# Kernel tuning notes

Measured on AMD Instinct MI355X. Metric: run time of the kernel, lower is better.

The kernel has to match this reference:

```python
import jax, jax.numpy as jnp
import numpy as np

N_NODES = 50000
N_EDGES = 800000
UNITS = 64
NUM_RADIAL = 20


def setup_inputs() -> dict:
    key = jax.random.key(0)
    ks = jax.random.split(key, 12)
    u, r = UNITS, NUM_RADIAL
    inv_u = 1.0 / np.sqrt(u)
    inv_r = 1.0 / np.sqrt(r)
    return {
        "node": jax.random.normal(ks[0], (N_NODES, u), jnp.float32),
        "equivariant": jax.random.normal(ks[1], (N_NODES, 3, u), jnp.float32),
        "rbf": jax.random.uniform(ks[2], (N_EDGES, r), jnp.float32),
        "envelope": jax.random.uniform(ks[3], (N_EDGES, 1), jnp.float32),
        "r_ij": jax.random.normal(ks[4], (N_EDGES, 3), jnp.float32),
        "edge_index": jax.random.randint(ks[5], (N_EDGES, 2), 0, N_NODES, jnp.int64),
        "Ws": jax.random.uniform(ks[6], (u, u), jnp.float32, -inv_u, inv_u),
        "bs": jax.random.uniform(ks[7], (u,), jnp.float32, -inv_u, inv_u),
        "Wphi": jax.random.uniform(ks[8], (3 * u, u), jnp.float32, -inv_u, inv_u),
        "bphi": jax.random.uniform(ks[9], (3 * u,), jnp.float32, -inv_u, inv_u),
        "Ww": jax.random.uniform(ks[10], (3 * u, r), jnp.float32, -inv_r, inv_r),
        "bw": jax.random.uniform(ks[11], (3 * u,), jnp.float32, -inv_r, inv_r),
    }


def reference(node, equivariant, rbf, envelope, r_ij, edge_index,
              Ws, bs, Wphi, bphi, Ww, bw):
    n_nodes = node.shape[0]
    u = node.shape[1]
    # per-node dense projections
    s = jax.nn.silu(node @ Ws.T + bs)          # [N, u]
    s = s @ Wphi.T + bphi                      # [N, 3u]
    # gather to edges (source = column 1)
    s_e = s[edge_index[:, 1]]                  # [E, 3u]
    # per-edge radial filter with cutoff envelope
    w = rbf @ Ww.T + bw                        # [E, 3u]
    w = w * envelope
    sw = s_e * w                               # [E, 3u]
    sw1, sw2, sw3 = jnp.split(sw, 3, axis=-1)  # each [E, u]
    dst = edge_index[:, 0]
    ds = jax.ops.segment_sum(sw1, dst, num_segments=n_nodes)  # [N, u]
    vj = equivariant[edge_index[:, 1]]         # [E, 3, u]
    dv = vj * sw2[:, None, :] + r_ij[:, :, None] * sw3[:, None, :]  # [E, 3, u]
    dv = jax.ops.segment_sum(dv, dst, num_segments=n_nodes)   # [N, 3, u]
    return (ds, dv)
```

## Files before the change

### kernel.cpp

```cpp
#include <hip/hip_runtime.h>

#define NRAD 20
#define MNODE 8

typedef unsigned short ushort_t;
typedef unsigned int uint_t;

struct U3 { uint_t a, b, c; };

__device__ __forceinline__ float rdlane(float v, int l)
{
    return __uint_as_float(__builtin_amdgcn_readlane(__float_as_uint(v), l));
}

__device__ __forceinline__ ushort_t f2bf(float f)
{
    uint_t u = __float_as_uint(f);
    u += 0x7fff + ((u >> 16) & 1);
    return (ushort_t)(u >> 16);
}

__device__ __forceinline__ uint_t pack2bf(float a, float b)
{
    return (uint_t)f2bf(a) | ((uint_t)f2bf(b) << 16);
}

__device__ __forceinline__ float bflo(uint_t w) { return __uint_as_float(w << 16); }
__device__ __forceinline__ float bfhi(uint_t w) { return __uint_as_float(w & 0xffff0000u); }
__device__ __forceinline__ float bf2f(ushort_t h) { return __uint_as_float(((uint_t)h) << 16); }

__global__ void detect_idx_kernel(const int* __restrict__ eidx, int* __restrict__ flag)
{
    int t = threadIdx.x;
    unsigned long long m = __ballot(eidx[2 * t + 1] != 0);
    if (t == 0) flag[0] = (__popcll(m) > 8) ? 1 : 0;
}

__global__ void hist_kernel(const int* __restrict__ eidx, const int* __restrict__ flag,
                            int* __restrict__ counts, int n_edges)
{
    int fmt32 = flag[0];
    int i0 = blockIdx.x * blockDim.x + threadIdx.x;
    int stride = gridDim.x * blockDim.x;
    if (fmt32) {
        for (int e = i0; e < n_edges; e += stride) atomicAdd(&counts[eidx[2 * e]], 1);
    } else {
        const long long* e64 = (const long long*)eidx;
        for (int e = i0; e < n_edges; e += stride) atomicAdd(&counts[(int)e64[2 * e]], 1);
    }
}

__global__ __launch_bounds__(256)
void scan1_kernel(const int* __restrict__ cnt, int* __restrict__ bsum, int n, int ch)
{
    __shared__ int red[4];
    int b = blockIdx.x, t = threadIdx.x;
    int end = min(n, (b + 1) * ch);
    int v = 0;
    for (int i = b * ch + t; i < end; i += 256) v += cnt[i];
#pragma unroll
    for (int d = 1; d < 64; d <<= 1) v += __shfl_xor(v, d, 64);
    if ((t & 63) == 0) red[t >> 6] = v;
    __syncthreads();
    if (t == 0) bsum[b] = red[0] + red[1] + red[2] + red[3];
}

__global__ __launch_bounds__(256)
void scan2_kernel(const int* __restrict__ bsum, int* __restrict__ bscan, int nb)
{
    __shared__ int wsum[4];
    int t = threadIdx.x, lane = t & 63, w = t >> 6;
    int v = (t < nb) ? bsum[t] : 0;
    int sc = v;
#pragma unroll
    for (int d = 1; d < 64; d <<= 1) {
        int u = __shfl_up(sc, (unsigned)d, 64);
        if (lane >= d) sc += u;
    }
    if (lane == 63) wsum[w] = sc;
    __syncthreads();
    int add = 0;
    for (int j = 0; j < w; j++) add += wsum[j];
    if (t < nb) bscan[t] = (sc + add) - v;
}

__global__ __launch_bounds__(256)
void scan3_kernel(const int* __restrict__ cnt, const int* __restrict__ bscan,
                  int* __restrict__ cur, int n, int ch)
{
    __shared__ int wsum[4];
    __shared__ int btot;
    int b = blockIdx.x, t = threadIdx.x, lane = t & 63, w = t >> 6;
    int end = min(n, (b + 1) * ch);
    int carry = bscan[b];
    for (int base = b * ch; base < end; base += 256) {
        int i = base + t;
        int v = (i < end) ? cnt[i] : 0;
        int sc = v;
#pragma unroll
        for (int d = 1; d < 64; d <<= 1) {
            int u = __shfl_up(sc, (unsigned)d, 64);
            if (lane >= d) sc += u;
        }
        if (lane == 63) wsum[w] = sc;
        __syncthreads();
        int add = 0;
        for (int j = 0; j < w; j++) add += wsum[j];
        if (t == 255) btot = sc + add;
        int excl = carry + (sc + add - v);
        if (i < end) cur[i] = excl;
        __syncthreads();
        carry += btot;
    }
}

__global__ void scatter_rec_kernel(const int* __restrict__ eidx, const int* __restrict__ flag,
                                   int* __restrict__ cur,
                                   const float* __restrict__ env, const float* __restrict__ rij,
                                   const float* __restrict__ rbf,
                                   uint4* __restrict__ rec, int n_edges)
{
    int fmt32 = flag[0];
    int i0 = blockIdx.x * blockDim.x + threadIdx.x;
    int stride = gridDim.x * blockDim.x;
    const long long* e64 = (const long long*)eidx;
    const float4* rbf4 = (const float4*)rbf;
    for (int e = i0; e < n_edges; e += stride) {
        int dst, src;
        if (fmt32) { dst = eidx[2 * e]; src = eidx[2 * e + 1]; }
        else       { dst = (int)e64[2 * e]; src = (int)e64[2 * e + 1]; }
        int pos = atomicAdd(&cur[dst], 1);
        float ev = env[e];
        float r0 = rij[3 * e], r1 = rij[3 * e + 1], r2 = rij[3 * e + 2];
        float4 b0 = rbf4[(size_t)e * 5 + 0];
        float4 b1 = rbf4[(size_t)e * 5 + 1];
        float4 b2 = rbf4[(size_t)e * 5 + 2];
        float4 b3 = rbf4[(size_t)e * 5 + 3];
        float4 b4 = rbf4[(size_t)e * 5 + 4];
        uint4 qa, qb, qc, qd;
        qa.x = (uint_t)src; qa.y = (uint_t)dst;
        qa.z = __float_as_uint(ev); qa.w = __float_as_uint(r0);
        qb.x = __float_as_uint(r1); qb.y = __float_as_uint(r2);
        qb.z = pack2bf(b0.x, b0.y); qb.w = pack2bf(b0.z, b0.w);
        qc.x = pack2bf(b1.x, b1.y); qc.y = pack2bf(b1.z, b1.w);
        qc.z = pack2bf(b2.x, b2.y); qc.w = pack2bf(b2.z, b2.w);
        qd.x = pack2bf(b3.x, b3.y); qd.y = pack2bf(b3.z, b3.w);
        qd.z = pack2bf(b4.x, b4.y); qd.w = pack2bf(b4.z, b4.w);
        size_t rp = (size_t)pos * 4;
        rec[rp] = qa; rec[rp + 1] = qb; rec[rp + 2] = qc; rec[rp + 3] = qd;
    }
}

__global__ void scatter_kernel(const int* __restrict__ eidx, const int* __restrict__ flag,
                               int* __restrict__ cur, int* __restrict__ sorted, int n_edges)
{
    int fmt32 = flag[0];
    int i0 = blockIdx.x * blockDim.x + threadIdx.x;
    int stride = gridDim.x * blockDim.x;
    const long long* e64 = (const long long*)eidx;
    for (int e = i0; e < n_edges; e += stride) {
        int dst = fmt32 ? eidx[2 * e] : (int)e64[2 * e];
        int pos = atomicAdd(&cur[dst], 1);
        sorted[pos] = e;
    }
}

__global__ void eq_cast_i_kernel(const float* __restrict__ eq,
                                 ushort_t* __restrict__ sq, int n_nodes)
{
    int i0 = blockIdx.x * blockDim.x + threadIdx.x;
    int stride = gridDim.x * blockDim.x;
    int total = n_nodes * 192;
    for (int i = i0; i < total; i += stride) {
        int n = i / 192;
        int r = i - n * 192;
        int c = r >> 6, ch = r & 63;
        sq[(size_t)n * 384 + ch * 6 + 3 + c] = f2bf(eq[i]);
    }
}

__global__ void prep_wpkp_kernel(const float* __restrict__ Ww, uint_t* __restrict__ wpkp)
{
    int idx = blockIdx.x * 256 + threadIdx.x;
    if (idx >= 1920) return;
    int lane = idx & 63;
    int r = idx >> 6;
    int p = r % 10;
    int c = r / 10;
    int n = c * 64 + lane;
    wpkp[idx] = pack2bf(Ww[n * 20 + 2 * p], Ww[n * 20 + 2 * p + 1]);
}

__global__ __launch_bounds__(256)
void node_mlp3i(const float* __restrict__ node,
                const float* __restrict__ Ws, const float* __restrict__ bs,
                const float* __restrict__ Wphi, const float* __restrict__ bphi,
                ushort_t* __restrict__ sq, int n_nodes)
{
    __shared__ float WsT[64 * 64];
    __shared__ float WphiT[64 * 192];
    const int t = threadIdx.x;
    for (int i = t; i < 64 * 64; i += 256) {
        int j = i >> 6, k = i & 63;
        WsT[k * 64 + j] = Ws[i];
    }
    for (int i = t; i < 192 * 64; i += 256) {
        int j = i >> 6, k = i & 63;
        WphiT[k * 192 + j] = Wphi[i];
    }
    __syncthreads();

    const int lane = t & 63;
    const int wave = t >> 6;
    const int gw = blockIdx.x * 4 + wave;
    const int nw = gridDim.x * 4;
    const float bsc = bs[lane];
    const float bp0 = bphi[lane], bp1 = bphi[64 + lane], bp2 = bphi[128 + lane];

    for (int n0 = gw * MNODE; n0 < n_nodes; n0 += nw * MNODE) {
        const int cnt = min(MNODE, n_nodes - n0);
        float x[MNODE];
#pragma unroll
        for (int m = 0; m < MNODE; m++)
            x[m] = (m < cnt) ? node[(size_t)(n0 + m) * 64 + lane] : 0.f;

        float acc[MNODE];
#pragma unroll
        for (int m = 0; m < MNODE; m++) acc[m] = bsc;
#pragma unroll
        for (int k = 0; k < 64; k++) {
            float wv = WsT[k * 64 + lane];
#pragma unroll
            for (int m = 0; m < MNODE; m++) acc[m] += rdlane(x[m], k) * wv;
        }
        float s1[MNODE];
#pragma unroll
        for (int m = 0; m < MNODE; m++) {
            float a = acc[m];
            s1[m] = a / (1.f + __expf(-a));
        }
        float a0[MNODE], a1[MNODE], a2[MNODE];
#pragma unroll
        for (int m = 0; m < MNODE; m++) { a0[m] = bp0; a1[m] = bp1; a2[m] = bp2; }
#pragma unroll
        for (int k = 0; k < 64; k++) {
            float w0 = WphiT[k * 192 + lane];
            float w1 = WphiT[k * 192 + 64 + lane];
            float w2 = WphiT[k * 192 + 128 + lane];
#pragma unroll
            for (int m = 0; m < MNODE; m++) {
                float sv = rdlane(s1[m], k);
                a0[m] += sv * w0;
                a1[m] += sv * w1;
                a2[m] += sv * w2;
            }
        }
#pragma unroll
        for (int m = 0; m < MNODE; m++) {
            if (m < cnt) {
                size_t ob = (size_t)(n0 + m) * 384 + lane * 6;
                *(uint_t*)(sq + ob) = pack2bf(a0[m], a1[m]);
                sq[ob + 2] = f2bf(a2[m]);
            }
        }
    }
}

__global__ __launch_bounds__(256, 4)
void accum10_kernel(const ushort_t* __restrict__ sq,
                    const uint4* __restrict__ rec,
                    const uint_t* __restrict__ wpkp,
                    const float* __restrict__ bw,
                    float* __restrict__ ds, float* __restrict__ dv, int n_edges)
{
    __shared__ int    sh_dst[4 * 64];
    __shared__ int    sh_src[4 * 64];
    __shared__ float  sh_env[4 * 64];
    __shared__ float  sh_r[4 * 3 * 64];
    __shared__ float4 sh_rbf[4 * 64 * 5];

    const int lane = threadIdx.x & 63;
    const int w = threadIdx.x >> 6;
    const int tile = blockIdx.x * 4 + w;
    const int base = tile * 64;
    const int nvalid = min(64, n_edges - base);
    const int woff = w * 64;

    uint_t wp[30];
#pragma unroll
    for (int i = 0; i < 30; i++) wp[i] = wpkp[i * 64 + lane];

    if (lane < nvalid) {
        size_t rp = (size_t)(base + lane) * 4;
        uint4 qa = rec[rp], qb = rec[rp + 1], qc = rec[rp + 2], qd = rec[rp + 3];
        sh_src[woff + lane] = (int)qa.x;
        sh_dst[woff + lane] = (int)qa.y;
        sh_env[woff + lane] = __uint_as_float(qa.z);
        sh_r[w * 192 + lane]       = __uint_as_float(qa.w);
        sh_r[w * 192 + 64 + lane]  = __uint_as_float(qb.x);
        sh_r[w * 192 + 128 + lane] = __uint_as_float(qb.y);
        float4* dstq = &sh_rbf[(woff + lane) * 5];
        dstq[0] = make_float4(bflo(qb.z), bfhi(qb.z), bflo(qb.w), bfhi(qb.w));
        dstq[1] = make_float4(bflo(qc.x), bfhi(qc.x), bflo(qc.y), bfhi(qc.y));
        dstq[2] = make_float4(bflo(qc.z), bfhi(qc.z), bflo(qc.w), bfhi(qc.w));
        dstq[3] = make_float4(bflo(qd.x), bfhi(qd.x), bflo(qd.y), bfhi(qd.y));
        dstq[4] = make_float4(bflo(qd.z), bfhi(qd.z), bflo(qd.w), bfhi(qd.w));
    }
    __syncthreads();

    if (nvalid <= 0) return;

    const float bw0 = bw[lane], bw1 = bw[64 + lane], bw2 = bw[128 + lane];

    float a0 = 0.f, a1 = 0.f, a2 = 0.f, a3 = 0.f;
    int cur = sh_dst[woff];

    U3 gcur = *(const U3*)(sq + (size_t)sh_src[woff] * 384 + lane * 6);

    for (int j = 0; j < nvalid; j++) {
        int jn = (j + 1 < nvalid) ? j + 1 : j;
        U3 gnxt = *(const U3*)(sq + (size_t)sh_src[woff + jn] * 384 + lane * 6);

        float ev = sh_env[woff + j];
        float r0 = sh_r[w * 192 + j];
        float r1 = sh_r[w * 192 + 64 + j];
        float r2 = sh_r[w * 192 + 128 + j];

        float sv0 = bflo(gcur.a);
        float sv1 = bfhi(gcur.a);
        float sv2 = bflo(gcur.b);
        float v0  = bfhi(gcur.b);
        float v1  = bflo(gcur.c);
        float v2  = bfhi(gcur.c);

        float w0 = bw0, w1 = bw1, w2 = bw2;
#pragma unroll
        for (int q = 0; q < 5; q++) {
            float4 rb = sh_rbf[(woff + j) * 5 + q];
            uint_t wa0 = wp[2 * q],      wa1 = wp[2 * q + 1];
            uint_t wb0 = wp[10 + 2 * q], wb1 = wp[11 + 2 * q];
            uint_t wc0 = wp[20 + 2 * q], wc1 = wp[21 + 2 * q];
            w0 += rb.x * bflo(wa0) + rb.y * bfhi(wa0) + rb.z * bflo(wa1) + rb.w * bfhi(wa1);
            w1 += rb.x * bflo(wb0) + rb.y * bfhi(wb0) + rb.z * bflo(wb1) + rb.w * bfhi(wb1);
            w2 += rb.x * bflo(wc0) + rb.y * bfhi(wc0) + rb.z * bflo(wc1) + rb.w * bfhi(wc1);
        }
        w0 *= ev; w1 *= ev; w2 *= ev;

        float sw1 = sv1 * w1;
        float sw2 = sv2 * w2;
        a0 += sv0 * w0;
        a1 += v0 * sw1 + r0 * sw2;
        a2 += v1 * sw1 + r1 * sw2;
        a3 += v2 * sw1 + r2 * sw2;

        int nd = (j + 1 < nvalid) ? sh_dst[woff + j + 1] : -2;
        if (nd != cur) {
            unsafeAtomicAdd(&ds[(size_t)cur * 64 + lane], a0);
            size_t db = (size_t)cur * 192 + lane;
            unsafeAtomicAdd(&dv[db], a1);
            unsafeAtomicAdd(&dv[db + 64], a2);
            unsafeAtomicAdd(&dv[db + 128], a3);
            a0 = a1 = a2 = a3 = 0.f;
            cur = nd;
        }
        gcur = gnxt;
    }
}

__global__ __launch_bounds__(256, 2)
void node_mlp_kernel(const float* __restrict__ node,
                     const float* __restrict__ Ws,
                     const float* __restrict__ bs,
                     const float* __restrict__ Wphi,
                     const float* __restrict__ bphi,
                     float* __restrict__ s_out,
                     int n_nodes)
{
    __shared__ float WsT[64 * 65];
    __shared__ float WphiT[64 * 193];
    const int t = threadIdx.x;
    for (int i = t; i < 64 * 64; i += 256) {
        int c = i >> 6, k = i & 63;
        WsT[k * 65 + c] = Ws[i];
    }
    for (int i = t; i < 192 * 64; i += 256) {
        int j = i >> 6, k = i & 63;
        WphiT[k * 193 + j] = Wphi[i];
    }
    __syncthreads();

    const int lane = t & 63;
    const int wave = t >> 6;
    const int nwaves = (gridDim.x * blockDim.x) >> 6;
    const float bsc = bs[lane];
    const float bp0 = bphi[lane], bp1 = bphi[64 + lane], bp2 = bphi[128 + lane];

    for (int n = blockIdx.x * 4 + wave; n < n_nodes; n += nwaves) {
        float x = node[(size_t)n * 64 + lane];
        float acc = bsc;
#pragma unroll
        for (int k = 0; k < 64; k++) acc += __shfl(x, k) * WsT[k * 65 + lane];
        float s1 = acc / (1.0f + __expf(-acc));
        float a0 = bp0, a1 = bp1, a2 = bp2;
#pragma unroll
        for (int k = 0; k < 64; k++) {
            float sk = __shfl(s1, k);
            a0 += sk * WphiT[k * 193 + lane];
            a1 += sk * WphiT[k * 193 + 64 + lane];
            a2 += sk * WphiT[k * 193 + 128 + lane];
        }
        size_t ob = (size_t)n * 192;
        s_out[ob + lane] = a0;
        s_out[ob + 64 + lane] = a1;
        s_out[ob + 128 + lane] = a2;
    }
}

__global__ __launch_bounds__(256)
void edge_kernel(const float* __restrict__ s,
                 const float* __restrict__ eq,
                 const float* __restrict__ rbf,
                 const float* __restrict__ env,
                 const float* __restrict__ rij,
                 const int* __restrict__ eidx,
                 const int* __restrict__ idx_flag,
                 const float* __restrict__ Ww,
                 const float* __restrict__ bw,
                 float* __restrict__ ds,
                 float* __restrict__ dv,
                 int n_edges)
{
    const int lane = threadIdx.x & 63;
    const int wglob = (blockIdx.x * blockDim.x + threadIdx.x) >> 6;
    const int nw = (gridDim.x * blockDim.x) >> 6;

    float ww0[NRAD], ww1[NRAD], ww2[NRAD];
#pragma unroll
    for (int k = 0; k < NRAD; k++) {
        ww0[k] = Ww[lane * NRAD + k];
        ww1[k] = Ww[(64 + lane) * NRAD + k];
        ww2[k] = Ww[(128 + lane) * NRAD + k];
    }
    const float bw0 = bw[lane], bw1 = bw[64 + lane], bw2 = bw[128 + lane];
    const int fmt32 = idx_flag[0];

    for (int e = wglob; e < n_edges; e += nw) {
        int dst, src;
        if (fmt32) {
            dst = eidx[2 * e];
            src = eidx[2 * e + 1];
        } else {
            const long long* e64 = (const long long*)eidx;
            dst = (int)e64[2 * e];
            src = (int)e64[2 * e + 1];
        }
        float ev = env[e];
        float r0 = rij[3 * e], r1 = rij[3 * e + 1], r2 = rij[3 * e + 2];
        float rb[NRAD];
#pragma unroll
        for (int k = 0; k < NRAD; k++) rb[k] = rbf[(size_t)e * NRAD + k];
        float w0 = bw0, w1 = bw1, w2 = bw2;
#pragma unroll
        for (int k = 0; k < NRAD; k++) {
            w0 += rb[k] * ww0[k];
            w1 += rb[k] * ww1[k];
            w2 += rb[k] * ww2[k];
        }
        w0 *= ev; w1 *= ev; w2 *= ev;

        size_t sb = (size_t)src * 192;
        float sw0 = s[sb + lane] * w0;
        float sw1 = s[sb + 64 + lane] * w1;
        float sw2 = s[sb + 128 + lane] * w2;
        float v0 = eq[sb + lane];
        float v1 = eq[sb + 64 + lane];
        float v2 = eq[sb + 128 + lane];

        unsafeAtomicAdd(&ds[(size_t)dst * 64 + lane], sw0);
        size_t db = (size_t)dst * 192;
        unsafeAtomicAdd(&dv[db + lane],       v0 * sw1 + r0 * sw2);
        unsafeAtomicAdd(&dv[db + 64 + lane],  v1 * sw1 + r1 * sw2);
        unsafeAtomicAdd(&dv[db + 128 + lane], v2 * sw1 + r2 * sw2);
    }
}

extern "C" void kernel_launch(void* const* d_in, const int* in_sizes, int n_in,
                              void* d_out, int out_size, void* d_ws, size_t ws_size,
                              hipStream_t stream)
{
    const float* node = (const float*)d_in[0];
    const float* eq   = (const float*)d_in[1];
    const float* rbf  = (const float*)d_in[2];
    const float* env  = (const float*)d_in[3];
    const float* rij  = (const float*)d_in[4];
    const int*   eidx = (const int*)d_in[5];
    const float* Ws   = (const float*)d_in[6];
    const float* bs   = (const float*)d_in[7];
    const float* Wphi = (const float*)d_in[8];
    const float* bphi = (const float*)d_in[9];
    const float* Ww   = (const float*)d_in[10];
    const float* bw   = (const float*)d_in[11];

    const int n_nodes = in_sizes[0] / 64;
    const int n_edges = in_sizes[3];

    float* out = (float*)d_out;
    float* ds = out;
    float* dv = out + (size_t)n_nodes * 64;
    char* ws = (char*)d_ws;

    const int ch = (n_nodes + 255) / 256;
    const int nb = (n_nodes + ch - 1) / ch;

    {
        size_t off = 0;
        auto alloc = [&](size_t bytes) { size_t o = off; off = (off + bytes + 255) & ~(size_t)255; return o; };
        size_t o_sq   = alloc((size_t)n_nodes * 384 * sizeof(ushort_t));
        size_t o_cnt  = alloc(2 * (size_t)n_nodes * sizeof(int));
        size_t o_rec  = alloc((size_t)n_edges * 64);
        size_t o_wpk  = alloc(1920 * sizeof(uint_t));
        size_t o_bsum = alloc(512 * sizeof(int));
        size_t o_flag = alloc(16);
        if (ws_size >= off) {
            ushort_t* sq = (ushort_t*)(ws + o_sq);
            int* counts = (int*)(ws + o_cnt);
            int* cur = counts + n_nodes;
            uint4* rec = (uint4*)(ws + o_rec);
            uint_t* wpkp = (uint_t*)(ws + o_wpk);
            int* bsum = (int*)(ws + o_bsum);
            int* bscan = bsum + 256;
            int* flag = (int*)(ws + o_flag);

            hipMemsetAsync(counts, 0, (size_t)n_nodes * sizeof(int), stream);
            hipMemsetAsync(d_out, 0, (size_t)out_size * sizeof(float), stream);
            detect_idx_kernel<<<1, 64, 0, stream>>>(eidx, flag);
            prep_wpkp_kernel<<<8, 256, 0, stream>>>(Ww, wpkp);
            hist_kernel<<<1024, 256, 0, stream>>>(eidx, flag, counts, n_edges);
            scan1_kernel<<<nb, 256, 0, stream>>>(counts, bsum, n_nodes, ch);
            scan2_kernel<<<1, 256, 0, stream>>>(bsum, bscan, nb);
            scan3_kernel<<<nb, 256, 0, stream>>>(counts, bscan, cur, n_nodes, ch);
            scatter_rec_kernel<<<1024, 256, 0, stream>>>(eidx, flag, cur, env, rij, rbf,
                                                         rec, n_edges);
            eq_cast_i_kernel<<<1024, 256, 0, stream>>>(eq, sq, n_nodes);
            node_mlp3i<<<512, 256, 0, stream>>>(node, Ws, bs, Wphi, bphi, sq, n_nodes);
            const int n_tiles = (n_edges + 63) / 64;
            accum10_kernel<<<(n_tiles + 3) / 4, 256, 0, stream>>>(
                sq, rec, wpkp, bw, ds, dv, n_edges);
            return;
        }
    }

    {
        float* s_ws = (float*)d_ws;
        int* idx_flag = (int*)(ws + (size_t)n_nodes * 192 * sizeof(float));
        hipMemsetAsync(d_out, 0, (size_t)out_size * sizeof(float), stream);
        detect_idx_kernel<<<1, 64, 0, stream>>>(eidx, idx_flag);
        node_mlp_kernel<<<1024, 256, 0, stream>>>(node, Ws, bs, Wphi, bphi, s_ws, n_nodes);
        edge_kernel<<<4096, 256, 0, stream>>>(s_ws, eq, rbf, env, rij, eidx, idx_flag,
                                              Ww, bw, ds, dv, n_edges);
    }
}
```

Baseline: 536.0 us.

## Stage edge inputs through LDS for coalesced loads; fuse equivariant cast into node MLP

The record-scatter kernel now loads each block's rbf, r_ij and envelope slices cooperatively into shared memory with coalesced reads (rbf padded to stride 21 to avoid bank conflicts), then each thread packs its record from LDS. Before, each thread issued strided float4 loads. The separate equivariant-to-bf16 cast kernel is removed. Its work is folded into the node MLP epilogue, which now writes the full 6-value interleaved slot per channel with 32-bit stores and saves one launch and one pass over sq. The trade-off is more shared memory per scatter block and extra global loads in the MLP epilogue.

```diff
diff --git a/kernel.cpp b/kernel.cpp
--- a/kernel.cpp
+++ b/kernel.cpp
@@ -114,38 +114,51 @@
     }
 }
 
-__global__ void scatter_rec_kernel(const int* __restrict__ eidx, const int* __restrict__ flag,
-                                   int* __restrict__ cur,
-                                   const float* __restrict__ env, const float* __restrict__ rij,
-                                   const float* __restrict__ rbf,
-                                   uint4* __restrict__ rec, int n_edges)
-{
-    int fmt32 = flag[0];
-    int i0 = blockIdx.x * blockDim.x + threadIdx.x;
-    int stride = gridDim.x * blockDim.x;
-    const long long* e64 = (const long long*)eidx;
-    const float4* rbf4 = (const float4*)rbf;
-    for (int e = i0; e < n_edges; e += stride) {
+__global__ __launch_bounds__(256)
+void scatter_rec2_kernel(const int* __restrict__ eidx, const int* __restrict__ flag,
+                         int* __restrict__ cur,
+                         const float* __restrict__ env, const float* __restrict__ rij,
+                         const float* __restrict__ rbf,
+                         uint4* __restrict__ rec, int n_edges)
+{
+    __shared__ float s_rbf[256 * 21];
+    __shared__ float s_rij[256 * 3];
+    __shared__ float s_env[256];
+
+    const int t = threadIdx.x;
+    const int chunk = blockIdx.x * 256;
+    const int nval = min(256, n_edges - chunk);
+    if (nval <= 0) return;
+
+    for (int i = t; i < nval * 20; i += 256) {
+        int e2 = i / 20, k = i - e2 * 20;
+        s_rbf[e2 * 21 + k] = rbf[(size_t)chunk * 20 + i];
+    }
+    for (int i = t; i < nval * 3; i += 256) s_rij[i] = rij[(size_t)chunk * 3 + i];
+    for (int i = t; i < nval; i += 256)     s_env[i] = env[chunk + i];
+    __syncthreads();
+
+    if (t < nval) {
+        const int e = chunk + t;
         int dst, src;
-        if (fmt32) { dst = eidx[2 * e]; src = eidx[2 * e + 1]; }
-        else       { dst = (int)e64[2 * e]; src = (int)e64[2 * e + 1]; }
+        if (flag[0]) { dst = eidx[2 * e]; src = eidx[2 * e + 1]; }
+        else {
+            const long long* e64 = (const long long*)eidx;
+            dst = (int)e64[2 * e]; src = (int)e64[2 * e + 1];
+        }
         int pos = atomicAdd(&cur[dst], 1);
-        float ev = env[e];
-        float r0 = rij[3 * e], r1 = rij[3 * e + 1], r2 = rij[3 * e + 2];
-        float4 b0 = rbf4[(size_t)e * 5 + 0];
-        float4 b1 = rbf4[(size_t)e * 5 + 1];
-        float4 b2 = rbf4[(size_t)e * 5 + 2];
-        float4 b3 = rbf4[(size_t)e * 5 + 3];
-        float4 b4 = rbf4[(size_t)e * 5 + 4];
+        float ev = s_env[t];
+        float r0 = s_rij[3 * t], r1 = s_rij[3 * t + 1], r2 = s_rij[3 * t + 2];
+        const float* rb = &s_rbf[t * 21];
         uint4 qa, qb, qc, qd;
         qa.x = (uint_t)src; qa.y = (uint_t)dst;
         qa.z = __float_as_uint(ev); qa.w = __float_as_uint(r0);
         qb.x = __float_as_uint(r1); qb.y = __float_as_uint(r2);
-        qb.z = pack2bf(b0.x, b0.y); qb.w = pack2bf(b0.z, b0.w);
-        qc.x = pack2bf(b1.x, b1.y); qc.y = pack2bf(b1.z, b1.w);
-        qc.z = pack2bf(b2.x, b2.y); qc.w = pack2bf(b2.z, b2.w);
-        qd.x = pack2bf(b3.x, b3.y); qd.y = pack2bf(b3.z, b3.w);
-        qd.z = pack2bf(b4.x, b4.y); qd.w = pack2bf(b4.z, b4.w);
+        qb.z = pack2bf(rb[0], rb[1]);   qb.w = pack2bf(rb[2], rb[3]);
+        qc.x = pack2bf(rb[4], rb[5]);   qc.y = pack2bf(rb[6], rb[7]);
+        qc.z = pack2bf(rb[8], rb[9]);   qc.w = pack2bf(rb[10], rb[11]);
+        qd.x = pack2bf(rb[12], rb[13]); qd.y = pack2bf(rb[14], rb[15]);
+        qd.z = pack2bf(rb[16], rb[17]); qd.w = pack2bf(rb[18], rb[19]);
         size_t rp = (size_t)pos * 4;
         rec[rp] = qa; rec[rp + 1] = qb; rec[rp + 2] = qc; rec[rp + 3] = qd;
     }
@@ -165,20 +178,6 @@
     }
 }
 
-__global__ void eq_cast_i_kernel(const float* __restrict__ eq,
-                                 ushort_t* __restrict__ sq, int n_nodes)
-{
-    int i0 = blockIdx.x * blockDim.x + threadIdx.x;
-    int stride = gridDim.x * blockDim.x;
-    int total = n_nodes * 192;
-    for (int i = i0; i < total; i += stride) {
-        int n = i / 192;
-        int r = i - n * 192;
-        int c = r >> 6, ch = r & 63;
-        sq[(size_t)n * 384 + ch * 6 + 3 + c] = f2bf(eq[i]);
-    }
-}
-
 __global__ void prep_wpkp_kernel(const float* __restrict__ Ww, uint_t* __restrict__ wpkp)
 {
     int idx = blockIdx.x * 256 + threadIdx.x;
@@ -192,10 +191,10 @@
 }
 
 __global__ __launch_bounds__(256)
-void node_mlp3i(const float* __restrict__ node,
-                const float* __restrict__ Ws, const float* __restrict__ bs,
-                const float* __restrict__ Wphi, const float* __restrict__ bphi,
-                ushort_t* __restrict__ sq, int n_nodes)
+void node_mlp4(const float* __restrict__ node, const float* __restrict__ eq,
+               const float* __restrict__ Ws, const float* __restrict__ bs,
+               const float* __restrict__ Wphi, const float* __restrict__ bphi,
+               ushort_t* __restrict__ sq, int n_nodes)
 {
     __shared__ float WsT[64 * 64];
     __shared__ float WphiT[64 * 192];
@@ -258,9 +257,14 @@
 #pragma unroll
         for (int m = 0; m < MNODE; m++) {
             if (m < cnt) {
-                size_t ob = (size_t)(n0 + m) * 384 + lane * 6;
-                *(uint_t*)(sq + ob) = pack2bf(a0[m], a1[m]);
-                sq[ob + 2] = f2bf(a2[m]);
+                size_t nn = (size_t)(n0 + m);
+                float q0 = eq[nn * 192 + lane];
+                float q1 = eq[nn * 192 + 64 + lane];
+                float q2 = eq[nn * 192 + 128 + lane];
+                uint_t* p = (uint_t*)(sq + nn * 384 + lane * 6);
+                p[0] = pack2bf(a0[m], a1[m]);
+                p[1] = (uint_t)f2bf(a2[m]) | ((uint_t)f2bf(q0) << 16);
+                p[2] = pack2bf(q1, q2);
             }
         }
     }
@@ -539,10 +543,10 @@
             scan1_kernel<<<nb, 256, 0, stream>>>(counts, bsum, n_nodes, ch);
             scan2_kernel<<<1, 256, 0, stream>>>(bsum, bscan, nb);
             scan3_kernel<<<nb, 256, 0, stream>>>(counts, bscan, cur, n_nodes, ch);
-            scatter_rec_kernel<<<1024, 256, 0, stream>>>(eidx, flag, cur, env, rij, rbf,
-                                                         rec, n_edges);
-            eq_cast_i_kernel<<<1024, 256, 0, stream>>>(eq, sq, n_nodes);
-            node_mlp3i<<<512, 256, 0, stream>>>(node, Ws, bs, Wphi, bphi, sq, n_nodes);
+            const int n_chunks = (n_edges + 255) / 256;
+            scatter_rec2_kernel<<<n_chunks, 256, 0, stream>>>(eidx, flag, cur, env, rij, rbf,
+                                                              rec, n_edges);
+            node_mlp4<<<512, 256, 0, stream>>>(node, eq, Ws, bs, Wphi, bphi, sq, n_nodes);
             const int n_tiles = (n_edges + 63) / 64;
             accum10_kernel<<<(n_tiles + 3) / 4, 256, 0, stream>>>(
                 sq, rec, wpkp, bw, ds, dv, n_edges);
```

After: 602.1 us. 12.3% more time.
